# Optimization experiments

Hardware: AMD Instinct MI355X
Metric: run time of the kernel (lower is better)

Reference implementation:

```python
import jax, jax.numpy as jnp
import numpy as np

NFIELD = 40

def setup_inputs() -> dict:
    key = jax.random.key(0)
    ks = jax.random.split(key, 7)
    B, F, E, A = 1024, NFIELD, 128, 128
    s = 1.0 / np.sqrt(E)
    return {
        "x": jax.random.normal(ks[0], (B, F, E), dtype=jnp.float32),
        "attn_w_w": jax.random.normal(ks[1], (A, E), dtype=jnp.float32) * s,
        "attn_w_b": jax.random.normal(ks[2], (A,), dtype=jnp.float32) * s,
        "attn_h_w": jax.random.normal(ks[3], (1, A), dtype=jnp.float32) * s,
        "attn_h_b": jax.random.normal(ks[4], (1,), dtype=jnp.float32) * s,
        "attn_p_w": jax.random.normal(ks[5], (1, E), dtype=jnp.float32) * s,
        "attn_p_b": jax.random.normal(ks[6], (1,), dtype=jnp.float32) * s,
    }

def reference(x, attn_w_w, attn_w_b, attn_h_w, attn_h_b, attn_p_w, attn_p_b):
    # x: [B, F, E]; pairwise field interactions over upper-triangular (i<j) pairs
    nfield = x.shape[1]
    vi, vj = np.triu_indices(nfield, k=1)  # static index arrays, P = F*(F-1)/2
    hp = x[:, vi, :] * x[:, vj, :]                                   # [B, P, E]
    aw = jax.nn.relu(jnp.einsum('bpe,ae->bpa', hp, attn_w_w) + attn_w_b)  # [B, P, A]
    scores = jnp.einsum('bpa,oa->bpo', aw, attn_h_w) + attn_h_b          # [B, P, 1]
    attn = jax.nn.softmax(scores, axis=1)                                # softmax over pairs
    afm = jnp.sum(attn * hp, axis=1)                                     # [B, E]
    out = jnp.einsum('be,oe->bo', afm, attn_p_w) + attn_p_b              # [B, 1]
    return out.squeeze(1)                                                # [B]
```

## Files before the change

### kernel.cpp

```cpp
#include <hip/hip_runtime.h>

#define NF 40
#define NE 128
#define NA 128
#define NP 780
#define NPT 784
#define NMT 49
#define XS_LD 132
#define G_LD 44

typedef short short8 __attribute__((ext_vector_type(8)));
typedef float floatx4 __attribute__((ext_vector_type(4)));

__device__ __forceinline__ unsigned cvt_pk_bf16(float lo, float hi) {
    unsigned r;
    asm("v_cvt_pk_bf16_f32 %0, %1, %2" : "=v"(r) : "v"(lo), "v"(hi));
    return r;
}

__device__ __forceinline__ float rowsum16(float x) {
    x += __int_as_float(__builtin_amdgcn_update_dpp(0, __float_as_int(x), 0x121, 0xf, 0xf, true));
    x += __int_as_float(__builtin_amdgcn_update_dpp(0, __float_as_int(x), 0x122, 0xf, 0xf, true));
    x += __int_as_float(__builtin_amdgcn_update_dpp(0, __float_as_int(x), 0x124, 0xf, 0xf, true));
    x += __int_as_float(__builtin_amdgcn_update_dpp(0, __float_as_int(x), 0x128, 0xf, 0xf, true));
    return x;
}

__global__ __launch_bounds__(256)
void afm_prep_kernel(const float* __restrict__ wg,
                     unsigned short* __restrict__ wbf,
                     int* __restrict__ ijg)
{
    const int t = blockIdx.x * 256 + threadIdx.x;
    if (t < NA * NE / 4) {
        float4 v = *(const float4*)(wg + t * 4);
        uint2 pk;
        pk.x = cvt_pk_bf16(v.x, v.y);
        pk.y = cvt_pk_bf16(v.z, v.w);
        *(uint2*)(wbf + t * 4) = pk;
    }
    if (t < NPT) {
        int v = 0;
        if (t < NP) {
            int i = 0, rem = t;
            while (rem >= (NF - 1 - i)) { rem -= (NF - 1 - i); ++i; }
            v = (i << 8) | (i + 1 + rem);
        }
        ijg[t] = v;
    }
}

__global__ __launch_bounds__(256, 2)
void afm_fused_kernel(const float* __restrict__ xg,
                      const unsigned short* __restrict__ wbf,
                      const int* __restrict__ ijg,
                      const float* __restrict__ wbg,
                      const float* __restrict__ hg,
                      const float* __restrict__ pwg,
                      const float* __restrict__ pbg,
                      float* __restrict__ out)
{
    __shared__ float xs[NF][XS_LD];
    __shared__ float sc[NPT];
    __shared__ int   ij[NPT];
    __shared__ float G[NF][G_LD];
    __shared__ float afmp[4][NE];
    __shared__ float red_max[4], red_sum[4], red_out[4];

    const int tid  = threadIdx.x;
    const int b    = blockIdx.x;
    const int lane = tid & 63;
    const int wid  = tid >> 6;
    const int col  = lane & 15;
    const int quad = (lane >> 4) & 3;

    const float* xb = xg + (size_t)b * (NF * NE);
    for (int t = tid; t < NF * (NE / 4); t += 256) {
        int row = t >> 5, c = (t & 31) * 4;
        float4 v = *(const float4*)(xb + row * NE + c);
        *(float4*)&xs[row][c] = v;
    }
    if (tid < NPT / 4) {
        *(int4*)&ij[tid * 4] = ((const int4*)ijg)[tid];
    }
    float wbr[8], hr[8];
#pragma unroll
    for (int n = 0; n < 8; ++n) {
        wbr[n] = wbg[n * 16 + col];
        hr[n]  = hg[n * 16 + col];
    }
    short8 bfrag[8][4];
#pragma unroll
    for (int n = 0; n < 8; ++n)
#pragma unroll
        for (int k = 0; k < 4; ++k)
            bfrag[n][k] = *(const short8*)(wbf + (n * 16 + col) * NE + k * 32 + quad * 8);
    __syncthreads();

    for (int mt = wid; mt < NMT; mt += 4) {
        const int p0 = mt * 16;
        const int v  = ij[p0 + col];
        const float* xip = &xs[(v >> 8) & 255][0];
        const float* xjp = &xs[v & 255][0];

        floatx4 acc[8];
#pragma unroll
        for (int n = 0; n < 8; ++n)
            acc[n] = (floatx4){wbr[n], wbr[n], wbr[n], wbr[n]};

#pragma unroll
        for (int k = 0; k < 4; ++k) {
            const int koff = k * 32 + quad * 8;
            float4 i0 = *(const float4*)(xip + koff);
            float4 i1 = *(const float4*)(xip + koff + 4);
            float4 j0 = *(const float4*)(xjp + koff);
            float4 j1 = *(const float4*)(xjp + koff + 4);
            union { short8 s; unsigned u[4]; } af;
            af.u[0] = cvt_pk_bf16(i0.x * j0.x, i0.y * j0.y);
            af.u[1] = cvt_pk_bf16(i0.z * j0.z, i0.w * j0.w);
            af.u[2] = cvt_pk_bf16(i1.x * j1.x, i1.y * j1.y);
            af.u[3] = cvt_pk_bf16(i1.z * j1.z, i1.w * j1.w);
#pragma unroll
            for (int n = 0; n < 8; ++n)
                acc[n] = __builtin_amdgcn_mfma_f32_16x16x32_bf16(af.s, bfrag[n][k], acc[n], 0, 0, 0);
        }

        float ps[4] = {0.f, 0.f, 0.f, 0.f};
#pragma unroll
        for (int n = 0; n < 8; ++n) {
#pragma unroll
            for (int r = 0; r < 4; ++r)
                ps[r] += fmaxf(acc[n][r], 0.f) * hr[n];
        }
#pragma unroll
        for (int r = 0; r < 4; ++r) ps[r] = rowsum16(ps[r]);
        if (col == 0) {
#pragma unroll
            for (int r = 0; r < 4; ++r) {
                int p = p0 + quad * 4 + r;
                if (p < NP) sc[p] = ps[r];
            }
        }
    }
    __syncthreads();

    float m = -1e30f;
    for (int p = tid; p < NP; p += 256) m = fmaxf(m, sc[p]);
#pragma unroll
    for (int off = 1; off < 64; off <<= 1) m = fmaxf(m, __shfl_xor(m, off));
    if (lane == 0) red_max[wid] = m;
    __syncthreads();
    const float M = fmaxf(fmaxf(red_max[0], red_max[1]), fmaxf(red_max[2], red_max[3]));

    float s = 0.f;
    for (int p = tid; p < NP; p += 256) {
        float e = __expf(sc[p] - M);
        sc[p] = e;
        s += e;
    }
#pragma unroll
    for (int off = 1; off < 64; off <<= 1) s += __shfl_xor(s, off);
    if (lane == 0) red_sum[wid] = s;
    __syncthreads();

    for (int p = tid; p < NP; p += 256) {
        int v = ij[p];
        float w = sc[p];
        G[(v >> 8) & 255][v & 255] = w;
        G[v & 255][(v >> 8) & 255] = w;
    }
    if (tid < NF) G[tid][tid] = 0.f;
    __syncthreads();

    {
        const int e2 = lane * 2;
        float2 xc[NF];
#pragma unroll
        for (int j = 0; j < NF; ++j) xc[j] = *(const float2*)&xs[j][e2];

        float a0 = 0.f, a1 = 0.f;
#pragma unroll
        for (int ii = 0; ii < 10; ++ii) {
            const int i = wid * 10 + ii;
            float y0 = 0.f, y1 = 0.f;
#pragma unroll
            for (int jj = 0; jj < 10; ++jj) {
                float4 g = *(const float4*)&G[i][jj * 4];
                y0 += g.x * xc[jj * 4 + 0].x;  y1 += g.x * xc[jj * 4 + 0].y;
                y0 += g.y * xc[jj * 4 + 1].x;  y1 += g.y * xc[jj * 4 + 1].y;
                y0 += g.z * xc[jj * 4 + 2].x;  y1 += g.z * xc[jj * 4 + 2].y;
                y0 += g.w * xc[jj * 4 + 3].x;  y1 += g.w * xc[jj * 4 + 3].y;
            }
            float2 xi = *(const float2*)&xs[i][e2];
            a0 += xi.x * y0;
            a1 += xi.y * y1;
        }
        *(float2*)&afmp[wid][e2] = make_float2(a0 * 0.5f, a1 * 0.5f);
    }
    __syncthreads();

    float vv = 0.f;
    if (tid < NE) {
        float a = afmp[0][tid] + afmp[1][tid] + afmp[2][tid] + afmp[3][tid];
        vv = a * pwg[tid];
    }
#pragma unroll
    for (int off = 1; off < 64; off <<= 1) vv += __shfl_xor(vv, off);
    if (lane == 0) red_out[wid] = vv;
    __syncthreads();
    if (tid == 0) {
        float S   = red_sum[0] + red_sum[1] + red_sum[2] + red_sum[3];
        float tot = red_out[0] + red_out[1] + red_out[2] + red_out[3];
        out[b] = tot / S + pbg[0];
    }
}

extern "C" void kernel_launch(void* const* d_in, const int* in_sizes, int n_in,
                              void* d_out, int out_size, void* d_ws, size_t ws_size,
                              hipStream_t stream) {
    const float* xg  = (const float*)d_in[0];
    const float* wg  = (const float*)d_in[1];
    const float* wbg = (const float*)d_in[2];
    const float* hg  = (const float*)d_in[3];
    const float* pwg = (const float*)d_in[5];
    const float* pbg = (const float*)d_in[6];
    const int B = in_sizes[0] / (NF * NE);

    unsigned short* wbf = (unsigned short*)d_ws;
    int* ijg = (int*)((char*)d_ws + NA * NE * sizeof(unsigned short));

    afm_prep_kernel<<<16, 256, 0, stream>>>(wg, wbf, ijg);
    afm_fused_kernel<<<B, 256, 0, stream>>>(xg, wbf, ijg, wbg, hg, pwg, pbg, (float*)d_out);
}
```

Before: 122.4 us.

## Process two batch samples per block to amortize weight fragment loads

Result: no change. 121.0 us (-1.2%).

```diff
diff --git a/kernel.cpp b/kernel.cpp
--- a/kernel.cpp
+++ b/kernel.cpp
@@ -6,6 +6,7 @@
 #define NP 780
 #define NPT 784
 #define NMT 49
+#define NT2 98
 #define XS_LD 132
 #define G_LD 44
 
@@ -60,12 +61,12 @@
                       const float* __restrict__ pbg,
                       float* __restrict__ out)
 {
-    __shared__ float xs[NF][XS_LD];
-    __shared__ float sc[NPT];
+    __shared__ float xs[2][NF][XS_LD];
+    __shared__ float sc[2][NPT];
     __shared__ int   ij[NPT];
-    __shared__ float G[NF][G_LD];
-    __shared__ float afmp[4][NE];
-    __shared__ float red_max[4], red_sum[4], red_out[4];
+    __shared__ float G[2][NF][G_LD];
+    __shared__ float afmp[2][2][NE];
+    __shared__ float red_max4[2][4], red_sum[2][2], red_out[2][2];
 
     const int tid  = threadIdx.x;
     const int b    = blockIdx.x;
@@ -74,14 +75,20 @@
     const int col  = lane & 15;
     const int quad = (lane >> 4) & 3;
 
-    const float* xb = xg + (size_t)b * (NF * NE);
-    for (int t = tid; t < NF * (NE / 4); t += 256) {
-        int row = t >> 5, c = (t & 31) * 4;
-        float4 v = *(const float4*)(xb + row * NE + c);
-        *(float4*)&xs[row][c] = v;
+    const float* xb = xg + (size_t)b * (2 * NF * NE);
+    for (int t = tid; t < 2 * NF * (NE / 4); t += 256) {
+        int s   = (t >= 1280) ? 1 : 0;
+        int rem = t - s * 1280;
+        int row = rem >> 5, c = (rem & 31) * 4;
+        float4 v = *(const float4*)(xb + s * (NF * NE) + row * NE + c);
+        *(float4*)&xs[s][row][c] = v;
     }
     if (tid < NPT / 4) {
         *(int4*)&ij[tid * 4] = ((const int4*)ijg)[tid];
+    }
+    if (tid < 2 * NF) {
+        int s = tid / NF, f = tid - s * NF;
+        G[s][f][f] = 0.f;
     }
     float wbr[8], hr[8];
 #pragma unroll
@@ -97,11 +104,14 @@
             bfrag[n][k] = *(const short8*)(wbf + (n * 16 + col) * NE + k * 32 + quad * 8);
     __syncthreads();
 
-    for (int mt = wid; mt < NMT; mt += 4) {
+    float mloc0 = -1e30f, mloc1 = -1e30f;
+    for (int g = wid; g < NT2; g += 4) {
+        const int s  = (g >= NMT) ? 1 : 0;
+        const int mt = g - s * NMT;
         const int p0 = mt * 16;
         const int v  = ij[p0 + col];
-        const float* xip = &xs[(v >> 8) & 255][0];
-        const float* xjp = &xs[v & 255][0];
+        const float* xip = &xs[s][(v >> 8) & 255][0];
+        const float* xjp = &xs[s][v & 255][0];
 
         floatx4 acc[8];
 #pragma unroll
@@ -115,14 +125,14 @@
             float4 i1 = *(const float4*)(xip + koff + 4);
             float4 j0 = *(const float4*)(xjp + koff);
             float4 j1 = *(const float4*)(xjp + koff + 4);
-            union { short8 s; unsigned u[4]; } af;
+            union { short8 s8; unsigned u[4]; } af;
             af.u[0] = cvt_pk_bf16(i0.x * j0.x, i0.y * j0.y);
             af.u[1] = cvt_pk_bf16(i0.z * j0.z, i0.w * j0.w);
             af.u[2] = cvt_pk_bf16(i1.x * j1.x, i1.y * j1.y);
             af.u[3] = cvt_pk_bf16(i1.z * j1.z, i1.w * j1.w);
 #pragma unroll
             for (int n = 0; n < 8; ++n)
-                acc[n] = __builtin_amdgcn_mfma_f32_16x16x32_bf16(af.s, bfrag[n][k], acc[n], 0, 0, 0);
+                acc[n] = __builtin_amdgcn_mfma_f32_16x16x32_bf16(af.s8, bfrag[n][k], acc[n], 0, 0, 0);
         }
 
         float ps[4] = {0.f, 0.f, 0.f, 0.f};
@@ -134,84 +144,87 @@
         }
 #pragma unroll
         for (int r = 0; r < 4; ++r) ps[r] = rowsum16(ps[r]);
+
+        float pm = -1e30f;
+#pragma unroll
+        for (int r = 0; r < 4; ++r)
+            pm = fmaxf(pm, (p0 + quad * 4 + r < NP) ? ps[r] : -1e30f);
+        if (s) mloc1 = fmaxf(mloc1, pm); else mloc0 = fmaxf(mloc0, pm);
+
         if (col == 0) {
 #pragma unroll
             for (int r = 0; r < 4; ++r) {
                 int p = p0 + quad * 4 + r;
-                if (p < NP) sc[p] = ps[r];
+                if (p < NP) sc[s][p] = ps[r];
             }
         }
     }
-    __syncthreads();
-
-    float m = -1e30f;
-    for (int p = tid; p < NP; p += 256) m = fmaxf(m, sc[p]);
-#pragma unroll
-    for (int off = 1; off < 64; off <<= 1) m = fmaxf(m, __shfl_xor(m, off));
-    if (lane == 0) red_max[wid] = m;
-    __syncthreads();
-    const float M = fmaxf(fmaxf(red_max[0], red_max[1]), fmaxf(red_max[2], red_max[3]));
-
-    float s = 0.f;
-    for (int p = tid; p < NP; p += 256) {
-        float e = __expf(sc[p] - M);
-        sc[p] = e;
-        s += e;
-    }
-#pragma unroll
-    for (int off = 1; off < 64; off <<= 1) s += __shfl_xor(s, off);
-    if (lane == 0) red_sum[wid] = s;
-    __syncthreads();
-
-    for (int p = tid; p < NP; p += 256) {
+#pragma unroll
+    for (int off = 1; off < 64; off <<= 1) {
+        mloc0 = fmaxf(mloc0, __shfl_xor(mloc0, off));
+        mloc1 = fmaxf(mloc1, __shfl_xor(mloc1, off));
+    }
+    if (lane == 0) { red_max4[0][wid] = mloc0; red_max4[1][wid] = mloc1; }
+    __syncthreads();
+
+    const int s    = wid >> 1;
+    const int lw   = wid & 1;
+    const int ltid = (lw << 6) | lane;
+    const float M = fmaxf(fmaxf(red_max4[s][0], red_max4[s][1]),
+                          fmaxf(red_max4[s][2], red_max4[s][3]));
+
+    float sum = 0.f;
+    for (int p = ltid; p < NP; p += 128) {
         int v = ij[p];
-        float w = sc[p];
-        G[(v >> 8) & 255][v & 255] = w;
-        G[v & 255][(v >> 8) & 255] = w;
-    }
-    if (tid < NF) G[tid][tid] = 0.f;
+        float e = __expf(sc[s][p] - M);
+        G[s][(v >> 8) & 255][v & 255] = e;
+        G[s][v & 255][(v >> 8) & 255] = e;
+        sum += e;
+    }
+#pragma unroll
+    for (int off = 1; off < 64; off <<= 1) sum += __shfl_xor(sum, off);
+    if (lane == 0) red_sum[s][lw] = sum;
     __syncthreads();
 
     {
         const int e2 = lane * 2;
         float2 xc[NF];
 #pragma unroll
-        for (int j = 0; j < NF; ++j) xc[j] = *(const float2*)&xs[j][e2];
+        for (int j = 0; j < NF; ++j) xc[j] = *(const float2*)&xs[s][j][e2];
 
         float a0 = 0.f, a1 = 0.f;
 #pragma unroll
-        for (int ii = 0; ii < 10; ++ii) {
-            const int i = wid * 10 + ii;
+        for (int ii = 0; ii < 20; ++ii) {
+            const int i = lw * 20 + ii;
             float y0 = 0.f, y1 = 0.f;
 #pragma unroll
             for (int jj = 0; jj < 10; ++jj) {
-                float4 g = *(const float4*)&G[i][jj * 4];
+                float4 g = *(const float4*)&G[s][i][jj * 4];
                 y0 += g.x * xc[jj * 4 + 0].x;  y1 += g.x * xc[jj * 4 + 0].y;
                 y0 += g.y * xc[jj * 4 + 1].x;  y1 += g.y * xc[jj * 4 + 1].y;
                 y0 += g.z * xc[jj * 4 + 2].x;  y1 += g.z * xc[jj * 4 + 2].y;
                 y0 += g.w * xc[jj * 4 + 3].x;  y1 += g.w * xc[jj * 4 + 3].y;
             }
-            float2 xi = *(const float2*)&xs[i][e2];
+            float2 xi = *(const float2*)&xs[s][i][e2];
             a0 += xi.x * y0;
             a1 += xi.y * y1;
         }
-        *(float2*)&afmp[wid][e2] = make_float2(a0 * 0.5f, a1 * 0.5f);
-    }
-    __syncthreads();
-
-    float vv = 0.f;
-    if (tid < NE) {
-        float a = afmp[0][tid] + afmp[1][tid] + afmp[2][tid] + afmp[3][tid];
-        vv = a * pwg[tid];
-    }
-#pragma unroll
-    for (int off = 1; off < 64; off <<= 1) vv += __shfl_xor(vv, off);
-    if (lane == 0) red_out[wid] = vv;
-    __syncthreads();
-    if (tid == 0) {
-        float S   = red_sum[0] + red_sum[1] + red_sum[2] + red_sum[3];
-        float tot = red_out[0] + red_out[1] + red_out[2] + red_out[3];
-        out[b] = tot / S + pbg[0];
+        *(float2*)&afmp[s][lw][e2] = make_float2(a0 * 0.5f, a1 * 0.5f);
+    }
+    __syncthreads();
+
+    {
+        float a  = afmp[s][0][ltid] + afmp[s][1][ltid];
+        float vv = a * pwg[ltid];
+#pragma unroll
+        for (int off = 1; off < 64; off <<= 1) vv += __shfl_xor(vv, off);
+        if (lane == 0) red_out[s][lw] = vv;
+    }
+    __syncthreads();
+    if ((tid & 127) == 0) {
+        float S   = red_sum[s][0] + red_sum[s][1];
+        float tot = red_out[s][0] + red_out[s][1];
+        out[2 * b + s] = tot / S + pbg[0];
     }
 }
 
@@ -230,5 +243,5 @@
     int* ijg = (int*)((char*)d_ws + NA * NE * sizeof(unsigned short));
 
     afm_prep_kernel<<<16, 256, 0, stream>>>(wg, wbf, ijg);
-    afm_fused_kernel<<<B, 256, 0, stream>>>(xg, wbf, ijg, wbg, hg, pwg, pbg, (float*)d_out);
-}
+    afm_fused_kernel<<<B / 2, 256, 0, stream>>>(xg, wbf, ijg, wbg, hg, pwg, pbg, (float*)d_out);
+}
```
